# Kernel optimization log

Hardware: AMD Instinct MI355X
Metric: run time of the kernel (lower is better)

## Reference

```python
import jax, jax.numpy as jnp
import numpy as np
from jax import lax

B, T, D, L, H, F = 2, 128, 256, 8, 4, 2048  # batch, time, dim, max_chunk_len, nhead, dim_feedforward
THRESH = 0.5


def setup_inputs() -> dict:
    key = jax.random.key(0)
    ks = jax.random.split(key, 12)
    s = 0.02
    nrm = lambda k, sh, sc=s: jax.random.normal(k, sh, jnp.float32) * sc
    return {
        "frames": jax.random.normal(ks[0], (B, T, D), jnp.float32),
        "cls_token": jax.random.normal(ks[1], (D,), jnp.float32),
        "Wq": nrm(ks[2], (D, D)), "bq": jnp.zeros((D,), jnp.float32),
        "Wk": nrm(ks[3], (D, D)), "bk": jnp.zeros((D,), jnp.float32),
        "Wv": nrm(ks[4], (D, D)), "bv": jnp.zeros((D,), jnp.float32),
        "Wo": nrm(ks[5], (D, D)), "bo": jnp.zeros((D,), jnp.float32),
        "ln1_g": jnp.ones((D,), jnp.float32), "ln1_b": jnp.zeros((D,), jnp.float32),
        "ln2_g": jnp.ones((D,), jnp.float32), "ln2_b": jnp.zeros((D,), jnp.float32),
        "W1": nrm(ks[6], (D, F)), "b1f": jnp.zeros((F,), jnp.float32),
        "W2": nrm(ks[7], (F, D)), "b2f": jnp.zeros((D,), jnp.float32),
        "We1": nrm(ks[8], (D, D)), "be1": jnp.zeros((D,), jnp.float32),
        "We2": jax.random.normal(ks[9], (D,), jnp.float32) * 0.1,
        "be2": jnp.zeros((), jnp.float32),
    }


def reference(frames, cls_token, Wq, bq, Wk, bk, Wv, bv, Wo, bo,
              ln1_g, ln1_b, ln2_g, ln2_b, W1, b1f, W2, b2f,
              We1, be1, We2, be2):
    """Dynamic chunker: for each start index i, grow window 1..L over frames[i:],
    run a pre-norm TransformerEncoderLayer on [CLS, window], stop at first
    p_eoc > THRESH (or window cap). Emits CLS encodings per chunk.
    Returns (chunks [B,T,D] zero-padded, counts [B])."""
    Bq, Tq, Dq = frames.shape
    dh = Dq // H
    scale = 1.0 / np.sqrt(dh).astype(np.float32)

    def ln(x, g, b):
        m = jnp.mean(x, -1, keepdims=True)
        v = jnp.var(x, -1, keepdims=True)
        return (x - m) * lax.rsqrt(v + 1e-5) * g + b

    def enc_cls(seq, kp):
        # seq: (1+L, D); kp: (1+L,) True = padded key. norm_first encoder layer.
        S = seq.shape[0]
        h = ln(seq, ln1_g, ln1_b)
        q = (h @ Wq + bq).reshape(S, H, dh)
        k = (h @ Wk + bk).reshape(S, H, dh)
        v = (h @ Wv + bv).reshape(S, H, dh)
        scores = jnp.einsum('qhd,khd->hqk', q, k) * scale
        scores = jnp.where(kp[None, None, :], -1e30, scores)
        a = jax.nn.softmax(scores, axis=-1)
        o = jnp.einsum('hqk,khd->qhd', a, v).reshape(S, Dq)
        x = seq + o @ Wo + bo
        h2 = ln(x, ln2_g, ln2_b)
        x = x + jax.nn.relu(h2 @ W1 + b1f) @ W2 + b2f
        return x[0]  # CLS position

    pos = jnp.arange(L)
    ls = jnp.arange(1, L + 1)

    def run(fpad):  # fpad: (T+L, D), one sample
        def step(i, _):
            win = lax.dynamic_slice(fpad, (i, 0), (L, Dq))           # frames[i:i+L] (zero-padded past T)
            seq = jnp.concatenate([cls_token[None, :], win], 0)     # (1+L, D)
            base_pad = (i + pos) >= Tq                               # positions past end of sequence
            kp = jnp.concatenate(
                [jnp.zeros((L, 1), bool),
                 (pos[None, :] >= ls[:, None]) | base_pad[None, :]], 1)  # (L, 1+L) one mask per candidate len
            enc = jax.vmap(enc_cls, in_axes=(None, 0))(seq, kp)      # (L, D) candidate CLS encodings
            p = jax.nn.sigmoid(jax.nn.relu(enc @ We1 + be1) @ We2 + be2)  # (L,) eoc probs
            lmax = jnp.clip(Tq - i, 1, L)
            stop = (p > THRESH) & (ls <= lmax)
            lstar = jnp.where(stop.any(), jnp.argmax(stop) + 1, lmax)
            active = i < Tq
            chunk = jnp.where(active, enc[lstar - 1], jnp.zeros((Dq,), seq.dtype))
            i_new = jnp.where(active, i + lstar.astype(i.dtype), i)
            return i_new, (chunk, active)

        _, (chunks, act) = lax.scan(step, jnp.int32(0), None, length=Tq)
        return chunks, act

    fpadded = jnp.pad(frames, ((0, 0), (0, L), (0, 0)))
    chunks, act = jax.vmap(run)(fpadded)
    counts = act.sum(-1).astype(jnp.int32)
    return chunks, counts
```

## Files before the change

### kernel.cpp

```cpp
#include <hip/hip_runtime.h>

#define DEV __device__ __forceinline__

constexpr int Bc = 2, Tc = 128, Dc = 256, Lc = 8, Hc = 4, DH = 64, Fc = 2048;
constexpr float EPS = 1e-5f, SCALE = 0.125f;
constexpr int NROWS = Bc * Tc * Lc;
constexpr int SLAB = NROWS * Dc;

constexpr int OFF_K     = 0;
constexpr int OFF_VWOH  = OFF_K + Bc * Tc * Dc;
constexpr int OFF_QCLS  = OFF_VWOH + Bc * Tc * Hc * Dc;
constexpr int OFF_KCLS  = OFF_QCLS + Dc;
constexpr int OFF_VWOHC = OFF_KCLS + Dc;
constexpr int OFF_X0    = OFF_VWOHC + Hc * Dc;
constexpr int OFF_ENC   = OFF_X0;
constexpr int OFF_H2    = OFF_X0 + SLAB;
constexpr int OFF_Z     = OFF_H2 + SLAB;

DEV int imin(int a, int b) { return a < b ? a : b; }

DEV float blockReduceSum(float v, float* red) {
#pragma unroll
  for (int off = 32; off; off >>= 1) v += __shfl_down(v, off, 64);
  const int lane = threadIdx.x & 63;
  const int w = threadIdx.x >> 6;
  __syncthreads();
  if (lane == 0) red[w] = v;
  __syncthreads();
  return red[0] + red[1] + red[2] + red[3];
}

__global__ __launch_bounds__(256) void k_prep(
    const float* __restrict__ frames, const float* __restrict__ cls,
    const float* __restrict__ Wq, const float* __restrict__ bq,
    const float* __restrict__ Wk, const float* __restrict__ bk,
    const float* __restrict__ Wv, const float* __restrict__ bv,
    const float* __restrict__ Wo,
    const float* __restrict__ g1, const float* __restrict__ b1,
    float* __restrict__ ws) {
  __shared__ float hsm[Dc];
  __shared__ float vsm[Dc];
  __shared__ float red[4];
  const int d = threadIdx.x;
  const int r = blockIdx.x;

  const float x = (r < Bc * Tc) ? frames[r * Dc + d] : cls[d];
  const float s = blockReduceSum(x, red);
  const float m = s * (1.0f / Dc);
  const float c = x - m;
  const float var = blockReduceSum(c * c, red) * (1.0f / Dc);
  hsm[d] = c * (1.0f / sqrtf(var + EPS)) * g1[d] + b1[d];
  __syncthreads();

  float ka = bk[d], va = bv[d];
  for (int c2 = 0; c2 < Dc; ++c2) {
    const float h = hsm[c2];
    ka = fmaf(h, Wk[c2 * Dc + d], ka);
    va = fmaf(h, Wv[c2 * Dc + d], va);
  }
  if (r < Bc * Tc) ws[OFF_K + r * Dc + d] = ka;
  else             ws[OFF_KCLS + d] = ka;
  vsm[d] = va;
  __syncthreads();

#pragma unroll
  for (int hh = 0; hh < Hc; ++hh) {
    float acc = 0.f;
    for (int c2 = 0; c2 < DH; ++c2)
      acc = fmaf(vsm[hh * DH + c2], Wo[(hh * DH + c2) * Dc + d], acc);
    if (r < Bc * Tc) ws[OFF_VWOH + r * (Hc * Dc) + hh * Dc + d] = acc;
    else             ws[OFF_VWOHC + hh * Dc + d] = acc;
  }
  if (r == Bc * Tc) {
    float qa = bq[d];
    for (int c2 = 0; c2 < Dc; ++c2) qa = fmaf(hsm[c2], Wq[c2 * Dc + d], qa);
    ws[OFF_QCLS + d] = qa;
  }
}

__global__ __launch_bounds__(256) void k_attn(
    const float* __restrict__ cls, const float* __restrict__ bo,
    const float* __restrict__ g2, const float* __restrict__ b2,
    float* __restrict__ ws) {
  const int wg = blockIdx.x;
  const int i = wg & (Tc - 1);
  const int d = threadIdx.x;
  const int lmax = imin(Tc - i, Lc);
  __shared__ float sv[Hc][Lc + 1];
  __shared__ float aP[Lc][Hc][Lc + 1];
  __shared__ __align__(16) float redA[Lc][4];
  __shared__ __align__(16) float redB[Lc][4];

  const int hh = d >> 6, lane = d & 63;
  {
    const float qv = ws[OFF_QCLS + hh * DH + lane];
    for (int j = 0; j <= Lc; ++j) {
      float p = 0.f;
      if (j == 0) p = qv * ws[OFF_KCLS + hh * DH + lane];
      else if (j - 1 < lmax) p = qv * ws[OFF_K + (wg + j - 1) * Dc + hh * DH + lane];
#pragma unroll
      for (int off = 32; off; off >>= 1) p += __shfl_down(p, off, 64);
      if (lane == 0) sv[hh][j] = p * SCALE;
    }
  }
  __syncthreads();

  if (d < Lc * Hc) {
    const int l = (d >> 2) + 1, h4 = d & 3;
    if (l <= lmax) {
      float mx = -1e30f;
      for (int j = 0; j <= l; ++j) mx = fmaxf(mx, sv[h4][j]);
      float den = 0.f;
      for (int j = 0; j <= l; ++j) den += expf(sv[h4][j] - mx);
      const float inv = 1.f / den;
      for (int j = 0; j <= l; ++j) aP[l - 1][h4][j] = expf(sv[h4][j] - mx) * inv;
    }
  }
  __syncthreads();

  float x0v[Lc];
  const float base = cls[d] + bo[d];
#pragma unroll
  for (int l = 0; l < Lc; ++l) x0v[l] = base;
  for (int j = 0; j <= lmax; ++j) {
    const float* vw = (j == 0) ? (ws + OFF_VWOHC)
                               : (ws + OFF_VWOH + (wg + j - 1) * (Hc * Dc));
    for (int h4 = 0; h4 < Hc; ++h4) {
      const float w = vw[h4 * Dc + d];
      const int lstart = (j == 0) ? 1 : j;
      for (int l = lstart; l <= lmax; ++l) x0v[l - 1] = fmaf(aP[l - 1][h4][j], w, x0v[l - 1]);
    }
  }

#pragma unroll
  for (int l = 0; l < Lc; ++l) {
    float p = x0v[l];
#pragma unroll
    for (int off = 32; off; off >>= 1) p += __shfl_down(p, off, 64);
    if (lane == 0) redA[l][hh] = p;
  }
  __syncthreads();
  float mean[Lc];
#pragma unroll
  for (int l = 0; l < Lc; ++l) {
    const float4 s4 = *(const float4*)redA[l];
    mean[l] = (s4.x + s4.y + s4.z + s4.w) * (1.f / Dc);
  }
#pragma unroll
  for (int l = 0; l < Lc; ++l) {
    const float cv = x0v[l] - mean[l];
    float p = cv * cv;
#pragma unroll
    for (int off = 32; off; off >>= 1) p += __shfl_down(p, off, 64);
    if (lane == 0) redB[l][hh] = p;
  }
  __syncthreads();

  const float g2d = g2[d], b2d = b2[d];
  for (int l = 1; l <= lmax; ++l) {
    const float4 s4 = *(const float4*)redB[l - 1];
    const float var = (s4.x + s4.y + s4.z + s4.w) * (1.f / Dc);
    const float rstd = 1.f / sqrtf(var + EPS);
    const float h2 = (x0v[l - 1] - mean[l - 1]) * rstd * g2d + b2d;
    const int rowc = wg * Lc + l - 1;
    ws[OFF_X0 + rowc * Dc + d] = x0v[l - 1];
    ws[OFF_H2 + rowc * Dc + d] = h2;
  }
  for (int l = lmax + 1; l <= Lc; ++l) {
    const int rowc = wg * Lc + l - 1;
    ws[OFF_X0 + rowc * Dc + d] = 0.f;
    ws[OFF_H2 + rowc * Dc + d] = 0.f;
  }
}

__global__ __launch_bounds__(512) void k_ffn(
    const float* __restrict__ W1, const float* __restrict__ b1f,
    const float* __restrict__ W2, const float* __restrict__ b2f,
    const float* __restrict__ We1, const float* __restrict__ be1,
    const float* __restrict__ We2, const float* __restrict__ be2,
    float* __restrict__ ws) {
  const int r0 = blockIdx.x * 8;
  const int tid = threadIdx.x;
  const int wv = tid >> 6, lane = tid & 63;
  __shared__ float ts[8][1024];
  __shared__ float h2s[8][256];
  __shared__ float encs[8][256];
  __shared__ float zred[8][4];

  *(float4*)&h2s[wv][lane * 4] =
      *(const float4*)&ws[OFF_H2 + (r0 + wv) * Dc + lane * 4];
  __syncthreads();

  float u[8][4];
#pragma unroll
  for (int r = 0; r < 8; ++r) { u[r][0] = 0.f; u[r][1] = 0.f; u[r][2] = 0.f; u[r][3] = 0.f; }

  for (int half = 0; half < 2; ++half) {
    const int fg = half * 1024 + tid * 2;
    float t[8][2];
    {
      const float2 bb = *(const float2*)&b1f[fg];
#pragma unroll
      for (int r = 0; r < 8; ++r) { t[r][0] = bb.x; t[r][1] = bb.y; }
    }
    for (int c = 0; c < Dc; c += 4) {
      float2 wv1[4];
#pragma unroll
      for (int k = 0; k < 4; ++k) wv1[k] = *(const float2*)&W1[(c + k) * Fc + fg];
#pragma unroll
      for (int r = 0; r < 8; ++r) {
        const float4 h = *(const float4*)&h2s[r][c];
        const float hv[4] = {h.x, h.y, h.z, h.w};
#pragma unroll
        for (int k = 0; k < 4; ++k) {
          t[r][0] = fmaf(hv[k], wv1[k].x, t[r][0]);
          t[r][1] = fmaf(hv[k], wv1[k].y, t[r][1]);
        }
      }
    }
    __syncthreads();
#pragma unroll
    for (int r = 0; r < 8; ++r) {
      float2 v; v.x = fmaxf(t[r][0], 0.f); v.y = fmaxf(t[r][1], 0.f);
      *(float2*)&ts[r][tid * 2] = v;
    }
    __syncthreads();

    for (int kk = 0; kk < 128; kk += 4) {
      const int kl = wv * 128 + kk;
      const int kg = half * 1024 + kl;
      float4 wv2[4];
#pragma unroll
      for (int k = 0; k < 4; ++k)
        wv2[k] = *(const float4*)&W2[(kg + k) * Dc + lane * 4];
#pragma unroll
      for (int r = 0; r < 8; ++r) {
        const float4 h = *(const float4*)&ts[r][kl];
        const float hv[4] = {h.x, h.y, h.z, h.w};
#pragma unroll
        for (int k = 0; k < 4; ++k) {
          u[r][0] = fmaf(hv[k], wv2[k].x, u[r][0]);
          u[r][1] = fmaf(hv[k], wv2[k].y, u[r][1]);
          u[r][2] = fmaf(hv[k], wv2[k].z, u[r][2]);
          u[r][3] = fmaf(hv[k], wv2[k].w, u[r][3]);
        }
      }
    }
    __syncthreads();
  }

  float* redb = &ts[0][0];
  if (wv < 4) {
#pragma unroll
    for (int r = 0; r < 8; ++r) {
      float4 v; v.x = u[r][0]; v.y = u[r][1]; v.z = u[r][2]; v.w = u[r][3];
      *(float4*)&redb[(wv * 8 + r) * 256 + lane * 4] = v;
    }
  }
  __syncthreads();
  if (wv >= 4) {
#pragma unroll
    for (int r = 0; r < 8; ++r) {
      float4 p = *(float4*)&redb[((wv - 4) * 8 + r) * 256 + lane * 4];
      p.x += u[r][0]; p.y += u[r][1]; p.z += u[r][2]; p.w += u[r][3];
      *(float4*)&redb[((wv - 4) * 8 + r) * 256 + lane * 4] = p;
    }
  }
  __syncthreads();

  {
    const int r = wv, d4 = lane * 4;
    float4 s = *(const float4*)&redb[(0 * 8 + r) * 256 + d4];
    const float4 s1 = *(const float4*)&redb[(1 * 8 + r) * 256 + d4];
    const float4 s2 = *(const float4*)&redb[(2 * 8 + r) * 256 + d4];
    const float4 s3 = *(const float4*)&redb[(3 * 8 + r) * 256 + d4];
    s.x = ((s.x + s1.x) + s2.x) + s3.x;
    s.y = ((s.y + s1.y) + s2.y) + s3.y;
    s.z = ((s.z + s1.z) + s2.z) + s3.z;
    s.w = ((s.w + s1.w) + s2.w) + s3.w;
    const float4 x0 = *(const float4*)&ws[OFF_X0 + (r0 + r) * Dc + d4];
    const float4 bb = *(const float4*)&b2f[d4];
    float4 e;
    e.x = (x0.x + s.x) + bb.x; e.y = (x0.y + s.y) + bb.y;
    e.z = (x0.z + s.z) + bb.z; e.w = (x0.w + s.w) + bb.w;
    *(float4*)&ws[OFF_ENC + (r0 + r) * Dc + d4] = e;
    *(float4*)&encs[r][d4] = e;
  }
  __syncthreads();

  {
    const int f = tid & 255;
    const int rh = tid >> 8;
    float g[4];
    const float be1f = be1[f];
#pragma unroll
    for (int rr = 0; rr < 4; ++rr) g[rr] = be1f;
    for (int c = 0; c < Dc; ++c) {
      const float w = We1[c * Dc + f];
#pragma unroll
      for (int rr = 0; rr < 4; ++rr) g[rr] = fmaf(encs[rh * 4 + rr][c], w, g[rr]);
    }
    const float w2 = We2[f];
#pragma unroll
    for (int rr = 0; rr < 4; ++rr) {
      float p = fmaxf(g[rr], 0.f) * w2;
#pragma unroll
      for (int off = 32; off; off >>= 1) p += __shfl_down(p, off, 64);
      if (lane == 0) zred[wv][rr] = p;
    }
  }
  __syncthreads();
  if (tid < 8) {
    const int r = tid;
    const int wb = (r < 4) ? 0 : 4;
    const int rl = r & 3;
    const float z = ((zred[wb + 0][rl] + zred[wb + 1][rl]) + zred[wb + 2][rl]) +
                    zred[wb + 3][rl];
    ws[OFF_Z + blockIdx.x * 8 + r] = z + be2[0];
  }
}

__global__ __launch_bounds__(256) void k_emit(float* __restrict__ ws, float* __restrict__ out) {
  const int b = blockIdx.x;
  const int tid = threadIdx.x;
  __shared__ int lst[Tc];
  __shared__ int path[Tc];
  __shared__ int cnt_s;
  if (tid < Tc) {
    const int i = tid;
    const int lmax = imin(Tc - i, Lc);
    const float* z = ws + OFF_Z + (b * Tc + i) * Lc;
    int ls = lmax;
    for (int l = 1; l <= lmax; ++l) {
      if (z[l - 1] > 0.f) { ls = l; break; }
    }
    lst[tid] = ls;
  }
  __syncthreads();
  if (tid < 64) {
    const int a0 = lst[tid], a1 = lst[64 + tid];
    int cur = 0, s = 0;
    while (cur < Tc) {
      const int l = (cur < 64) ? __shfl(a0, cur, 64) : __shfl(a1, cur - 64, 64);
      if (tid == 0) path[s] = cur * Lc + l - 1;
      ++s;
      cur += l;
    }
    if (tid == 0) cnt_s = s;
  }
  __syncthreads();
  const int c = cnt_s;
  for (int s0 = 0; s0 < Tc; s0 += 8) {
    float v[8];
#pragma unroll
    for (int k = 0; k < 8; ++k) {
      const int s = s0 + k;
      v[k] = (s < c) ? ws[OFF_ENC + (b * Tc * Lc + path[s]) * Dc + tid] : 0.f;
    }
#pragma unroll
    for (int k = 0; k < 8; ++k) out[(b * Tc + s0 + k) * Dc + tid] = v[k];
  }
  if (tid == 0) out[Bc * Tc * Dc + b] = (float)c;
}

extern "C" void kernel_launch(void* const* d_in, const int* in_sizes, int n_in,
                              void* d_out, int out_size, void* d_ws, size_t ws_size,
                              hipStream_t stream) {
  const float* frames = (const float*)d_in[0];
  const float* cls    = (const float*)d_in[1];
  const float* Wq     = (const float*)d_in[2];
  const float* bq     = (const float*)d_in[3];
  const float* Wk     = (const float*)d_in[4];
  const float* bk     = (const float*)d_in[5];
  const float* Wv     = (const float*)d_in[6];
  const float* bv     = (const float*)d_in[7];
  const float* Wo     = (const float*)d_in[8];
  const float* bo     = (const float*)d_in[9];
  const float* g1     = (const float*)d_in[10];
  const float* b1     = (const float*)d_in[11];
  const float* g2     = (const float*)d_in[12];
  const float* b2     = (const float*)d_in[13];
  const float* W1     = (const float*)d_in[14];
  const float* b1f    = (const float*)d_in[15];
  const float* W2     = (const float*)d_in[16];
  const float* b2f    = (const float*)d_in[17];
  const float* We1    = (const float*)d_in[18];
  const float* be1    = (const float*)d_in[19];
  const float* We2    = (const float*)d_in[20];
  const float* be2    = (const float*)d_in[21];
  float* ws = (float*)d_ws;
  float* out = (float*)d_out;

  k_prep<<<Bc * Tc + 1, 256, 0, stream>>>(frames, cls, Wq, bq, Wk, bk, Wv, bv, Wo, g1, b1, ws);
  k_attn<<<Bc * Tc, 256, 0, stream>>>(cls, bo, g2, b2, ws);
  k_ffn<<<NROWS / 8, 512, 0, stream>>>(W1, b1f, W2, b2f, We1, be1, We2, be2, ws);
  k_emit<<<Bc, 256, 0, stream>>>(ws, out);
}
```

Baseline: 253.1 us.

## Fuse attention and FFN kernels, keep x0/h2 in shared memory

Merges the attention/LN2 kernel and the FFN/EOC-head kernel into one 512-thread kernel, one block per start index. Each block handles its 8 candidate rows. The x0 and h2 intermediates now stay in shared memory instead of going through global workspace, which removes one launch and the slab write/read round-trip. In exchange, half the threads sit idle during the attention phase, and the block uses more shared memory, which may lower occupancy.

```diff
diff --git a/kernel.cpp b/kernel.cpp
--- a/kernel.cpp
+++ b/kernel.cpp
@@ -12,10 +12,8 @@
 constexpr int OFF_QCLS  = OFF_VWOH + Bc * Tc * Hc * Dc;
 constexpr int OFF_KCLS  = OFF_QCLS + Dc;
 constexpr int OFF_VWOHC = OFF_KCLS + Dc;
-constexpr int OFF_X0    = OFF_VWOHC + Hc * Dc;
-constexpr int OFF_ENC   = OFF_X0;
-constexpr int OFF_H2    = OFF_X0 + SLAB;
-constexpr int OFF_Z     = OFF_H2 + SLAB;
+constexpr int OFF_ENC   = OFF_VWOHC + Hc * Dc;
+constexpr int OFF_Z     = OFF_ENC + SLAB;
 
 DEV int imin(int a, int b) { return a < b ? a : b; }
 
@@ -78,21 +76,32 @@
   }
 }
 
-__global__ __launch_bounds__(256) void k_attn(
+__global__ __launch_bounds__(512) void k_fused(
     const float* __restrict__ cls, const float* __restrict__ bo,
     const float* __restrict__ g2, const float* __restrict__ b2,
+    const float* __restrict__ W1, const float* __restrict__ b1f,
+    const float* __restrict__ W2, const float* __restrict__ b2f,
+    const float* __restrict__ We1, const float* __restrict__ be1,
+    const float* __restrict__ We2, const float* __restrict__ be2,
     float* __restrict__ ws) {
   const int wg = blockIdx.x;
   const int i = wg & (Tc - 1);
-  const int d = threadIdx.x;
+  const int tid = threadIdx.x;
+  const int wv = tid >> 6, lane = tid & 63;
   const int lmax = imin(Tc - i, Lc);
+
+  __shared__ float ts[8][1024];
+  __shared__ float h2s[8][256];
+  __shared__ float x0s[8][256];
+  __shared__ float encs[8][256];
   __shared__ float sv[Hc][Lc + 1];
   __shared__ float aP[Lc][Hc][Lc + 1];
   __shared__ __align__(16) float redA[Lc][4];
   __shared__ __align__(16) float redB[Lc][4];
-
-  const int hh = d >> 6, lane = d & 63;
-  {
+  __shared__ float zred[8][4];
+
+  if (tid < 256) {
+    const int hh = tid >> 6;
     const float qv = ws[OFF_QCLS + hh * DH + lane];
     for (int j = 0; j <= Lc; ++j) {
       float p = 0.f;
@@ -105,8 +114,8 @@
   }
   __syncthreads();
 
-  if (d < Lc * Hc) {
-    const int l = (d >> 2) + 1, h4 = d & 3;
+  if (tid < Lc * Hc) {
+    const int l = (tid >> 2) + 1, h4 = tid & 3;
     if (l <= lmax) {
       float mx = -1e30f;
       for (int j = 0; j <= l; ++j) mx = fmaxf(mx, sv[h4][j]);
@@ -119,76 +128,63 @@
   __syncthreads();
 
   float x0v[Lc];
-  const float base = cls[d] + bo[d];
-#pragma unroll
-  for (int l = 0; l < Lc; ++l) x0v[l] = base;
-  for (int j = 0; j <= lmax; ++j) {
-    const float* vw = (j == 0) ? (ws + OFF_VWOHC)
-                               : (ws + OFF_VWOH + (wg + j - 1) * (Hc * Dc));
-    for (int h4 = 0; h4 < Hc; ++h4) {
-      const float w = vw[h4 * Dc + d];
-      const int lstart = (j == 0) ? 1 : j;
-      for (int l = lstart; l <= lmax; ++l) x0v[l - 1] = fmaf(aP[l - 1][h4][j], w, x0v[l - 1]);
-    }
-  }
-
-#pragma unroll
-  for (int l = 0; l < Lc; ++l) {
-    float p = x0v[l];
-#pragma unroll
-    for (int off = 32; off; off >>= 1) p += __shfl_down(p, off, 64);
-    if (lane == 0) redA[l][hh] = p;
-  }
-  __syncthreads();
+  if (tid < 256) {
+    const int d = tid;
+    const float base = cls[d] + bo[d];
+#pragma unroll
+    for (int l = 0; l < Lc; ++l) x0v[l] = base;
+    for (int j = 0; j <= lmax; ++j) {
+      const float* vwp = (j == 0) ? (ws + OFF_VWOHC)
+                                  : (ws + OFF_VWOH + (wg + j - 1) * (Hc * Dc));
+      for (int h4 = 0; h4 < Hc; ++h4) {
+        const float w = vwp[h4 * Dc + d];
+        const int lstart = (j == 0) ? 1 : j;
+        for (int l = lstart; l <= lmax; ++l) x0v[l - 1] = fmaf(aP[l - 1][h4][j], w, x0v[l - 1]);
+      }
+    }
+#pragma unroll
+    for (int l = 0; l < Lc; ++l) {
+      float p = x0v[l];
+#pragma unroll
+      for (int off = 32; off; off >>= 1) p += __shfl_down(p, off, 64);
+      if (lane == 0) redA[l][tid >> 6] = p;
+    }
+  }
+  __syncthreads();
+
   float mean[Lc];
-#pragma unroll
-  for (int l = 0; l < Lc; ++l) {
-    const float4 s4 = *(const float4*)redA[l];
-    mean[l] = (s4.x + s4.y + s4.z + s4.w) * (1.f / Dc);
-  }
-#pragma unroll
-  for (int l = 0; l < Lc; ++l) {
-    const float cv = x0v[l] - mean[l];
-    float p = cv * cv;
-#pragma unroll
-    for (int off = 32; off; off >>= 1) p += __shfl_down(p, off, 64);
-    if (lane == 0) redB[l][hh] = p;
-  }
-  __syncthreads();
-
-  const float g2d = g2[d], b2d = b2[d];
-  for (int l = 1; l <= lmax; ++l) {
-    const float4 s4 = *(const float4*)redB[l - 1];
-    const float var = (s4.x + s4.y + s4.z + s4.w) * (1.f / Dc);
-    const float rstd = 1.f / sqrtf(var + EPS);
-    const float h2 = (x0v[l - 1] - mean[l - 1]) * rstd * g2d + b2d;
-    const int rowc = wg * Lc + l - 1;
-    ws[OFF_X0 + rowc * Dc + d] = x0v[l - 1];
-    ws[OFF_H2 + rowc * Dc + d] = h2;
-  }
-  for (int l = lmax + 1; l <= Lc; ++l) {
-    const int rowc = wg * Lc + l - 1;
-    ws[OFF_X0 + rowc * Dc + d] = 0.f;
-    ws[OFF_H2 + rowc * Dc + d] = 0.f;
-  }
-}
-
-__global__ __launch_bounds__(512) void k_ffn(
-    const float* __restrict__ W1, const float* __restrict__ b1f,
-    const float* __restrict__ W2, const float* __restrict__ b2f,
-    const float* __restrict__ We1, const float* __restrict__ be1,
-    const float* __restrict__ We2, const float* __restrict__ be2,
-    float* __restrict__ ws) {
-  const int r0 = blockIdx.x * 8;
-  const int tid = threadIdx.x;
-  const int wv = tid >> 6, lane = tid & 63;
-  __shared__ float ts[8][1024];
-  __shared__ float h2s[8][256];
-  __shared__ float encs[8][256];
-  __shared__ float zred[8][4];
-
-  *(float4*)&h2s[wv][lane * 4] =
-      *(const float4*)&ws[OFF_H2 + (r0 + wv) * Dc + lane * 4];
+  if (tid < 256) {
+#pragma unroll
+    for (int l = 0; l < Lc; ++l) {
+      const float4 s4 = *(const float4*)redA[l];
+      mean[l] = (s4.x + s4.y + s4.z + s4.w) * (1.f / Dc);
+    }
+#pragma unroll
+    for (int l = 0; l < Lc; ++l) {
+      const float cv = x0v[l] - mean[l];
+      float p = cv * cv;
+#pragma unroll
+      for (int off = 32; off; off >>= 1) p += __shfl_down(p, off, 64);
+      if (lane == 0) redB[l][tid >> 6] = p;
+    }
+  }
+  __syncthreads();
+
+  if (tid < 256) {
+    const int d = tid;
+    const float g2d = g2[d], b2d = b2[d];
+    for (int l = 1; l <= lmax; ++l) {
+      const float4 s4 = *(const float4*)redB[l - 1];
+      const float var = (s4.x + s4.y + s4.z + s4.w) * (1.f / Dc);
+      const float rstd = 1.f / sqrtf(var + EPS);
+      h2s[l - 1][d] = (x0v[l - 1] - mean[l - 1]) * rstd * g2d + b2d;
+      x0s[l - 1][d] = x0v[l - 1];
+    }
+    for (int l = lmax + 1; l <= Lc; ++l) {
+      h2s[l - 1][d] = 0.f;
+      x0s[l - 1][d] = 0.f;
+    }
+  }
   __syncthreads();
 
   float u[8][4];
@@ -278,12 +274,12 @@
     s.y = ((s.y + s1.y) + s2.y) + s3.y;
     s.z = ((s.z + s1.z) + s2.z) + s3.z;
     s.w = ((s.w + s1.w) + s2.w) + s3.w;
-    const float4 x0 = *(const float4*)&ws[OFF_X0 + (r0 + r) * Dc + d4];
+    const float4 x0 = *(const float4*)&x0s[r][d4];
     const float4 bb = *(const float4*)&b2f[d4];
     float4 e;
     e.x = (x0.x + s.x) + bb.x; e.y = (x0.y + s.y) + bb.y;
     e.z = (x0.z + s.z) + bb.z; e.w = (x0.w + s.w) + bb.w;
-    *(float4*)&ws[OFF_ENC + (r0 + r) * Dc + d4] = e;
+    *(float4*)&ws[OFF_ENC + (wg * 8 + r) * Dc + d4] = e;
     *(float4*)&encs[r][d4] = e;
   }
   __syncthreads();
@@ -316,7 +312,7 @@
     const int rl = r & 3;
     const float z = ((zred[wb + 0][rl] + zred[wb + 1][rl]) + zred[wb + 2][rl]) +
                     zred[wb + 3][rl];
-    ws[OFF_Z + blockIdx.x * 8 + r] = z + be2[0];
+    ws[OFF_Z + wg * 8 + r] = z + be2[0];
   }
 }
 
@@ -392,7 +388,6 @@
   float* out = (float*)d_out;
 
   k_prep<<<Bc * Tc + 1, 256, 0, stream>>>(frames, cls, Wq, bq, Wk, bk, Wv, bv, Wo, g1, b1, ws);
-  k_attn<<<Bc * Tc, 256, 0, stream>>>(cls, bo, g2, b2, ws);
-  k_ffn<<<NROWS / 8, 512, 0, stream>>>(W1, b1f, W2, b2f, We1, be1, We2, be2, ws);
+  k_fused<<<Bc * Tc, 512, 0, stream>>>(cls, bo, g2, b2, W1, b1f, W2, b2f, We1, be1, We2, be2, ws);
   k_emit<<<Bc, 256, 0, stream>>>(ws, out);
 }
```

Measured after the change: 243.4 us. 3.8% less time.
